# Performance work log

Hardware: AMD Instinct MI355X
Metric: run time of the kernel (lower is better)

The kernel has to match this reference:

```python
import jax, jax.numpy as jnp
import numpy as np

B, C, H, W = 2, 128, 64, 64
CR4 = C // 4  # hidden width of linear_weight / bias branches
SOFTMAX_SCALE = 1.0


def _leaky(z):
    return jnp.where(z >= 0, z, 0.2 * z)


def _conv1x1(x, w, b):
    # x: [B,Ci,H,W], w: [Co,Ci], b: [Co]
    return jnp.einsum('oc,bchw->bohw', w, x) + b[None, :, None, None]


def setup_inputs() -> dict:
    key = jax.random.key(0)
    ks = jax.random.split(key, 16)
    def n(k, shape, s=0.05):
        return jax.random.normal(k, shape, jnp.float32) * s
    return {
        'x': jax.random.normal(ks[0], (B, C, H, W), jnp.float32),
        'value_w': n(ks[1], (C, C)), 'value_b': n(ks[2], (C,)),
        'query_w': n(ks[3], (C, C)), 'query_b': n(ks[4], (C,)),
        'lw1_w': n(ks[5], (CR4, C)), 'lw1_b': n(ks[6], (CR4,)),
        'lw2_w': n(ks[7], (1, CR4)), 'lw2_b': n(ks[8], (1,)),
        'bi1_w': n(ks[9], (CR4, C)), 'bi1_b': n(ks[10], (CR4,)),
        'bi2_w': n(ks[11], (1, CR4)), 'bi2_b': n(ks[12], (1,)),
        'lin_w': n(ks[13], (C, C, 3, 3)), 'lin_b': n(ks[14], (C,)),
    }


def reference(x, value_w, value_b, query_w, query_b,
              lw1_w, lw1_b, lw2_w, lw2_b,
              bi1_w, bi1_b, bi2_w, bi2_b,
              lin_w, lin_b):
    # value / query 1x1 projections
    x1 = _conv1x1(x, value_w, value_b)   # [B,C,H,W]
    x2 = _conv1x1(x, query_w, query_b)   # [B,C,H,W]
    # dynamic per-pixel weight / bias maps (two 1x1 convs + LeakyReLU)
    wei = _conv1x1(_leaky(_conv1x1(x2, lw1_w, lw1_b)), lw2_w, lw2_b)  # [B,1,H,W]
    bii = _conv1x1(_leaky(_conv1x1(x2, bi1_w, bi1_b)), bi2_w, bi2_b)  # [B,1,H,W]

    Bn, Cn, Hn, Wn = x.shape
    L = Hn * Wn  # one 1x1 patch per spatial location (ksize=1, stride=1)
    # query patches [B,L,C]; normalize each patch to (at least 1e-4) unit norm
    wq = x2.transpose(0, 2, 3, 1).reshape(Bn, L, Cn)
    wnorm = wq / jnp.maximum(jnp.linalg.norm(wq, axis=2, keepdims=True), 1e-4)
    # attention scores: per-sample conv2d(xi, wi_normed) == batched matmul
    yi = jnp.einsum('bchw,blc->blhw', x2, wnorm)  # [B,L,H,W]
    # sparse gating
    sparse = jax.nn.relu(yi - yi.mean(axis=1, keepdims=True) * wei + bii)
    sr = (sparse != 0.0).astype(yi.dtype)
    yi = yi * sparse
    yi = jax.nn.softmax(yi * SOFTMAX_SCALE, axis=1)
    yi = jnp.maximum(yi * sr, 1e-8)
    # reconstruct with value patches (conv_transpose2d with 1x1 kernels)
    raw = x1.transpose(0, 2, 3, 1).reshape(Bn, L, Cn)
    out = jnp.einsum('blhw,blc->bchw', yi, raw)  # / (ksize*ksize) == /1
    # final 3x3 conv + LeakyReLU + residual
    y = jax.lax.conv_general_dilated(out, lin_w, (1, 1), 'SAME',
                                     dimension_numbers=('NCHW', 'OIHW', 'NCHW'))
    y = _leaky(y + lin_b[None, :, None, None])
    return y + x
```

## Files before the change

kernel.cpp:

```cpp
#include <hip/hip_runtime.h>
#include <hip/hip_bf16.h>
#include <math.h>

#define BB 2
#define C 128
#define L 4096
#define CR4 32
#define RS 4

typedef unsigned short ushort_t;
typedef __attribute__((ext_vector_type(8))) short s16x8;
typedef __attribute__((ext_vector_type(4))) float f32x4;

__device__ inline float leaky(float z) { return (z >= 0.f) ? z : 0.2f * z; }

__device__ inline unsigned short f2bf(float f) {
    unsigned int u = __builtin_bit_cast(unsigned int, f);
    unsigned int r = (u + 0x7fffu + ((u >> 16) & 1u)) >> 16;
    return (unsigned short)r;
}
__device__ inline float bf2f(unsigned short b) {
    unsigned int u = ((unsigned int)b) << 16;
    return __builtin_bit_cast(float, u);
}
__device__ inline unsigned int cvtpk(float lo, float hi) {
    unsigned int r;
    asm("v_cvt_pk_bf16_f32 %0, %1, %2" : "=v"(r) : "v"(lo), "v"(hi));
    return r;
}

__global__ __launch_bounds__(256) void k_wcomp(
    const float* __restrict__ vw, const float* __restrict__ vb,
    const float* __restrict__ qw, const float* __restrict__ qb,
    const float* __restrict__ lw1w, const float* __restrict__ lw1b,
    const float* __restrict__ bi1w, const float* __restrict__ bi1b,
    ushort_t* __restrict__ WQV, float* __restrict__ biasv)
{
    const int mt = blockIdx.x;
    const int t = threadIdx.x;
    const int kk = t >> 6, lane = t & 63;
    const int row = mt * 16 + (lane & 15);
    const int k0 = kk * 32 + (lane >> 4) * 8;
    s16x8 v;
    if (row < 128) {
        #pragma unroll
        for (int j = 0; j < 8; ++j) v[j] = (short)f2bf(vw[row * 128 + k0 + j]);
    } else if (row < 256) {
        #pragma unroll
        for (int j = 0; j < 8; ++j) v[j] = (short)f2bf(qw[(row - 128) * 128 + k0 + j]);
    } else {
        const float* w1 = (row < 288) ? lw1w + (row - 256) * 128
                                      : bi1w + (row - 288) * 128;
        float acc[8] = {0.f, 0.f, 0.f, 0.f, 0.f, 0.f, 0.f, 0.f};
        #pragma unroll 2
        for (int k = 0; k < 128; ++k) {
            float wv_ = w1[k];
            const float* qr = qw + k * 128 + k0;
            #pragma unroll
            for (int j = 0; j < 8; ++j) acc[j] = fmaf(wv_, qr[j], acc[j]);
        }
        #pragma unroll
        for (int j = 0; j < 8; ++j) v[j] = (short)f2bf(acc[j]);
    }
    *(s16x8*)(WQV + ((size_t)(mt * 4 + kk) * 64 + lane) * 8) = v;

    if (t < 16) {
        int rr = mt * 16 + t;
        float bv;
        if (rr < 128) bv = vb[rr];
        else if (rr < 256) bv = qb[rr - 128];
        else {
            const float* w1 = (rr < 288) ? lw1w + (rr - 256) * 128
                                         : bi1w + (rr - 288) * 128;
            float a = (rr < 288) ? lw1b[rr - 256] : bi1b[rr - 288];
            for (int k = 0; k < 128; ++k) a = fmaf(w1[k], qb[k], a);
            bv = a;
        }
        biasv[rr] = bv;
    }
}

__global__ __launch_bounds__(256, 1) void k_proj2(
    const float* __restrict__ x, const ushort_t* __restrict__ WQV,
    const float* __restrict__ biasv,
    const float* __restrict__ lw2w, const float* __restrict__ lw2b,
    const float* __restrict__ bi2w, const float* __restrict__ bi2b,
    ushort_t* __restrict__ x2a, ushort_t* __restrict__ x1g,
    float* __restrict__ weiA, float* __restrict__ biiA, float* __restrict__ scA,
    float* __restrict__ cpart)
{
    __shared__ __align__(16) char smem[16384 + 1536];
    char* xT = smem;
    float* biasLDS = (float*)(smem + 16384);
    float* w2LDS = biasLDS + 320;

    const int t = threadIdx.x;
    const int blk = blockIdx.x;
    const int part = blockIdx.y;
    const int b = blk >> 6;
    const int p0 = (blk & 63) * 64;
    const int wv = t >> 6, lane = t & 63, n = lane & 15, g = lane >> 4;

    biasLDS[t] = biasv[t];
    if (t < 64) {
        biasLDS[256 + t] = biasv[256 + t];
        w2LDS[t] = (t < 32) ? lw2w[t] : bi2w[t - 32];
    }

    const int pl = t & 63, cg = t >> 6;
    const float* xb = x + (size_t)b * C * L + p0 + pl;
    #pragma unroll
    for (int i = 0; i < 16; ++i) {
        int c = cg * 32 + i * 2;
        float v0 = xb[(size_t)c * L];
        float v1 = xb[(size_t)(c + 1) * L];
        int slot = c >> 3;
        int offs = (c * 2) & 15;
        int byte = pl * 256 + (((slot ^ (pl & 15)) << 4) | offs);
        *(unsigned int*)(xT + byte) = cvtpk(v0, v1);
    }
    __syncthreads();

    const int brow = wv * 16 + n;
    const int p = p0 + wv * 16 + n;
    const size_t bL = (size_t)b * L;

    if (part == 0) {
        const int mtm[12] = {0, 1, 2, 3, 4, 5, 6, 7, 16, 17, 18, 19};
        f32x4 acc[12];
        #pragma unroll
        for (int i = 0; i < 12; ++i) acc[i] = (f32x4){0.f, 0.f, 0.f, 0.f};
        #pragma unroll
        for (int kk = 0; kk < 4; ++kk) {
            const s16x8 bfr = *(const s16x8*)(xT + brow * 256 + (((4 * kk + g) ^ n) << 4));
            #pragma unroll
            for (int i = 0; i < 12; ++i) {
                const s16x8 afr = *(const s16x8*)(WQV + ((size_t)(mtm[i] * 4 + kk) * 64 + lane) * 8);
                acc[i] = __builtin_amdgcn_mfma_f32_16x16x32_bf16(afr, bfr, acc[i], 0, 0, 0);
            }
        }
        #pragma unroll
        for (int i = 0; i < 12; ++i) {
            const f32x4 bv = *(const f32x4*)(biasLDS + mtm[i] * 16 + g * 4);
            acc[i][0] += bv[0]; acc[i][1] += bv[1];
            acc[i][2] += bv[2]; acc[i][3] += bv[3];
        }
        #pragma unroll
        for (int i = 0; i < 8; ++i)
            #pragma unroll
            for (int r = 0; r < 4; ++r)
                x1g[((size_t)b * C + i * 16 + g * 4 + r) * L + p] = f2bf(acc[i][r]);
        float pw = 0.f, pbb = 0.f;
        #pragma unroll
        for (int i = 8; i < 10; ++i)
            #pragma unroll
            for (int r = 0; r < 4; ++r)
                pw = fmaf(w2LDS[(i - 8) * 16 + g * 4 + r], leaky(acc[i][r]), pw);
        #pragma unroll
        for (int i = 10; i < 12; ++i)
            #pragma unroll
            for (int r = 0; r < 4; ++r)
                pbb = fmaf(w2LDS[32 + (i - 10) * 16 + g * 4 + r], leaky(acc[i][r]), pbb);
        pw += __shfl_xor(pw, 16, 64);  pw += __shfl_xor(pw, 32, 64);
        pbb += __shfl_xor(pbb, 16, 64); pbb += __shfl_xor(pbb, 32, 64);
        if (g == 0) {
            weiA[bL + p] = pw + lw2b[0];
            biiA[bL + p] = pbb + bi2b[0];
        }
    } else {
        f32x4 acc[8];
        #pragma unroll
        for (int i = 0; i < 8; ++i) acc[i] = (f32x4){0.f, 0.f, 0.f, 0.f};
        #pragma unroll
        for (int kk = 0; kk < 4; ++kk) {
            const s16x8 bfr = *(const s16x8*)(xT + brow * 256 + (((4 * kk + g) ^ n) << 4));
            #pragma unroll
            for (int i = 0; i < 8; ++i) {
                const s16x8 afr = *(const s16x8*)(WQV + ((size_t)((8 + i) * 4 + kk) * 64 + lane) * 8);
                acc[i] = __builtin_amdgcn_mfma_f32_16x16x32_bf16(afr, bfr, acc[i], 0, 0, 0);
            }
        }
        #pragma unroll
        for (int i = 0; i < 8; ++i) {
            const f32x4 bv = *(const f32x4*)(biasLDS + (8 + i) * 16 + g * 4);
            acc[i][0] += bv[0]; acc[i][1] += bv[1];
            acc[i][2] += bv[2]; acc[i][3] += bv[3];
        }
        float pn = 0.f;
        #pragma unroll
        for (int i = 0; i < 8; ++i)
            #pragma unroll
            for (int r = 0; r < 4; ++r) pn = fmaf(acc[i][r], acc[i][r], pn);
        pn += __shfl_xor(pn, 16, 64);
        pn += __shfl_xor(pn, 32, 64);
        float scv = fmaxf(sqrtf(pn), 1e-4f);
        float dinv = 1.f / scv;
        if (g == 0) scA[bL + p] = scv;
        #pragma unroll
        for (int i = 0; i < 8; ++i) {
            uint2 uu;
            uu.x = cvtpk(acc[i][0] * dinv, acc[i][1] * dinv);
            uu.y = cvtpk(acc[i][2] * dinv, acc[i][3] * dinv);
            *(uint2*)(x2a + (bL + p) * C + i * 16 + g * 4) = uu;
        }
        float sv[32];
        #pragma unroll
        for (int i = 0; i < 8; ++i)
            #pragma unroll
            for (int r = 0; r < 4; ++r)
                sv[i * 4 + r] = acc[i][r] * dinv;
        #pragma unroll
        for (int mask = 1; mask <= 8; mask <<= 1)
            #pragma unroll
            for (int i = 0; i < 32; ++i)
                sv[i] += __shfl_xor(sv[i], mask, 64);
        __syncthreads();
        float* sumsh = (float*)xT;
        if (n == 0) {
            #pragma unroll
            for (int i = 0; i < 32; ++i) {
                int ch = (i >> 2) * 16 + g * 4 + (i & 3);
                sumsh[wv * 128 + ch] = sv[i];
            }
        }
        __syncthreads();
        if (t < 128)
            cpart[(size_t)blk * 128 + t] =
                (sumsh[t] + sumsh[128 + t]) + (sumsh[256 + t] + sumsh[384 + t]);
    }
}

__global__ __launch_bounds__(128) void k_cb(
    const float* __restrict__ cpart, float* __restrict__ cbv)
{
    const int b = blockIdx.x, t = threadIdx.x;
    float s = 0.f;
    #pragma unroll 4
    for (int j = 0; j < 64; ++j) s += cpart[(size_t)(b * 64 + j) * 128 + t];
    cbv[b * 128 + t] = s * (1.f / (float)L);
}

__global__ __launch_bounds__(256, 2) void k_attn(
    const ushort_t* __restrict__ x2a, const ushort_t* __restrict__ x1g,
    const float* __restrict__ scA, const float* __restrict__ weiA,
    const float* __restrict__ biiA, const float* __restrict__ cbv,
    ushort_t* __restrict__ Opb, float* __restrict__ Mp, float* __restrict__ Zp)
{
    __shared__ __align__(16) char smem[73728];

    const int t = threadIdx.x;
    const int w = t >> 6, lane = t & 63, n = lane & 15, g = lane >> 4;
    char* Pw = smem + 65536 + w * 2048;

    const int blk = blockIdx.x;
    const int q = blk & (RS - 1);
    const int colt = (blk >> 2) & 63;
    const int b = blk >> 8;
    const int p = colt * 64 + w * 16 + n;
    const size_t bL = (size_t)b * L;

    const s16x8* qrow = (const s16x8*)(x2a + (bL + p) * C);
    const float scp = scA[bL + p];
    s16x8 bq[4];
    float dot = 0.f;
    #pragma unroll
    for (int kk = 0; kk < 4; ++kk) {
        s16x8 raw = qrow[kk * 4 + g];
        const float* cbp = cbv + b * 128 + kk * 32 + g * 8;
        s16x8 u;
        #pragma unroll
        for (int j = 0; j < 8; ++j) {
            float rv = bf2f((unsigned short)raw[j]) * scp;
            u[j] = (short)f2bf(rv);
            dot = fmaf(cbp[j], rv, dot);
        }
        bq[kk] = u;
    }
    dot += __shfl_xor(dot, 16, 64);
    dot += __shfl_xor(dot, 32, 64);
    const float tq = fmaf(weiA[bL + p], dot, -biiA[bL + p]);

    f32x4 Oacc[8];
    #pragma unroll
    for (int ct = 0; ct < 8; ++ct) Oacc[ct] = (f32x4){0.f, 0.f, 0.f, 0.f};
    float Mrun = 0.f, Zrun = 0.f;

    const int l0base = q * (L / RS);
    const char* x2src = (const char*)(x2a + (bL + l0base) * C);
    const char* x1src = (const char*)(x1g + (size_t)b * C * L);

    #define STAGE_X2(buf, tile_)                                                         \
        {   const char* sb = x2src + (size_t)(tile_) * 64 * 256;                          \
            _Pragma("unroll")                                                             \
            for (int rr = 0; rr < 4; ++rr) {                                              \
                int slot = rr * 256 + t;                                                  \
                int lrow = slot >> 4, uu = slot & 15;                                     \
                const char* gp = sb + lrow * 256 + (((uu ^ (lrow & 7))) << 4);            \
                char* lp = (buf) + ((rr * 256 + w * 64) << 4);                            \
                __builtin_amdgcn_global_load_lds(                                         \
                    (const __attribute__((address_space(1))) unsigned int*)gp,            \
                    (__attribute__((address_space(3))) unsigned int*)lp, 16, 0, 0);       \
            } }
    #define STAGE_X1(buf, l0_)                                                            \
        {   _Pragma("unroll")                                                             \
            for (int rr = 0; rr < 4; ++rr) {                                              \
                int slot = rr * 256 + t;                                                  \
                int cr = slot >> 3, uu = slot & 7;                                        \
                const char* gp = x1src + ((size_t)cr * L + (l0_) + ((uu ^ (cr & 7)) << 3)) * 2; \
                char* lp = (buf) + ((rr * 256 + w * 64) << 4);                            \
                __builtin_amdgcn_global_load_lds(                                         \
                    (const __attribute__((address_space(1))) unsigned int*)gp,            \
                    (__attribute__((address_space(3))) unsigned int*)lp, 16, 0, 0);       \
            } }

    char* Abuf0 = smem;          char* Abuf1 = smem + 16384;
    char* Xbuf0 = smem + 32768;  char* Xbuf1 = smem + 49152;

    STAGE_X2(Abuf0, 0);
    STAGE_X1(Xbuf0, l0base);
    __syncthreads();

    const int swz = n & 7;
    const int NT = L / RS / 64;

    #pragma unroll 1
    for (int tile = 0; tile < NT; ++tile) {
        char* Ab = (tile & 1) ? Abuf1 : Abuf0;
        char* Xb = (tile & 1) ? Xbuf1 : Xbuf0;
        if (tile + 1 < NT) {
            char* An = (tile & 1) ? Abuf0 : Abuf1;
            char* Xn = (tile & 1) ? Xbuf0 : Xbuf1;
            STAGE_X2(An, tile + 1);
            STAGE_X1(Xn, l0base + (tile + 1) * 64);
        }

        f32x4 s4[4];
        #pragma unroll
        for (int lt = 0; lt < 4; ++lt) s4[lt] = (f32x4){0.f, 0.f, 0.f, 0.f};
        __builtin_amdgcn_s_setprio(1);
        #pragma unroll
        for (int kk = 0; kk < 4; ++kk) {
            #pragma unroll
            for (int lt = 0; lt < 4; ++lt) {
                const s16x8 a = *(const s16x8*)(Ab + (16 * lt + n) * 256 +
                                                (((4 * kk + g) ^ swz) << 4));
                s4[lt] = __builtin_amdgcn_mfma_f32_16x16x32_bf16(a, bq[kk], s4[lt], 0, 0, 0);
            }
        }
        __builtin_amdgcn_s_setprio(0);

        float vv[16], sps[16];
        #pragma unroll
        for (int lt = 0; lt < 4; ++lt) {
            #pragma unroll
            for (int r = 0; r < 4; ++r) {
                float s = s4[lt][r];
                float sp = s - tq;
                sps[lt * 4 + r] = sp;
                vv[lt * 4 + r] = s * fmaxf(sp, 0.f);
            }
        }
        float tm[8];
        #pragma unroll
        for (int i = 0; i < 8; ++i) tm[i] = fmaxf(vv[2 * i], vv[2 * i + 1]);
        #pragma unroll
        for (int i = 0; i < 4; ++i) tm[i] = fmaxf(tm[2 * i], tm[2 * i + 1]);
        float tmax = fmaxf(fmaxf(tm[0], tm[1]), fmaxf(tm[2], tm[3]));
        tmax = fmaxf(tmax, __shfl_xor(tmax, 16, 64));
        tmax = fmaxf(tmax, __shfl_xor(tmax, 32, 64));

        if (!__all(tmax <= Mrun + 8.f)) {
            float Mn = fmaxf(Mrun, tmax);
            float so = __expf(Mrun - Mn);
            Mrun = Mn;
            Zrun *= so;
            #pragma unroll
            for (int ct = 0; ct < 8; ++ct) {
                Oacc[ct][0] *= so; Oacc[ct][1] *= so;
                Oacc[ct][2] *= so; Oacc[ct][3] *= so;
            }
        }

        #pragma unroll
        for (int lt = 0; lt < 4; ++lt) {
            float e0 = __expf(vv[lt * 4 + 0] - Mrun);
            float e1 = __expf(vv[lt * 4 + 1] - Mrun);
            float e2 = __expf(vv[lt * 4 + 2] - Mrun);
            float e3 = __expf(vv[lt * 4 + 3] - Mrun);
            Zrun += (e0 + e1) + (e2 + e3);
            float p0 = sps[lt * 4 + 0] > 0.f ? e0 : 0.f;
            float p1 = sps[lt * 4 + 1] > 0.f ? e1 : 0.f;
            float p2 = sps[lt * 4 + 2] > 0.f ? e2 : 0.f;
            float p3 = sps[lt * 4 + 3] > 0.f ? e3 : 0.f;
            int ulog = 2 * lt + (g >> 1);
            int byte = n * 128 + ((ulog ^ swz) << 4) + ((g & 1) << 3);
            uint2 uu;
            uu.x = cvtpk(p0, p1);
            uu.y = cvtpk(p2, p3);
            *(uint2*)(Pw + byte) = uu;
        }

        __builtin_amdgcn_s_setprio(1);
        #pragma unroll
        for (int kk2 = 0; kk2 < 2; ++kk2) {
            const s16x8 pb = *(const s16x8*)(Pw + n * 128 + (((4 * kk2 + g) ^ swz) << 4));
            #pragma unroll
            for (int ct = 0; ct < 8; ++ct) {
                const s16x8 a = *(const s16x8*)(Xb + (16 * ct + n) * 128 +
                                                (((4 * kk2 + g) ^ swz) << 4));
                Oacc[ct] = __builtin_amdgcn_mfma_f32_16x16x32_bf16(a, pb, Oacc[ct], 0, 0, 0);
            }
        }
        __builtin_amdgcn_s_setprio(0);
        __syncthreads();
    }
    #undef STAGE_X2
    #undef STAGE_X1

    float z = Zrun;
    z += __shfl_xor(z, 16, 64);
    z += __shfl_xor(z, 32, 64);

    const size_t sset = (size_t)(q * BB + b);
    ushort_t* ob = Opb + (sset * L + p) * C;
    #pragma unroll
    for (int ct = 0; ct < 8; ++ct) {
        uint2 uu;
        uu.x = cvtpk(Oacc[ct][0], Oacc[ct][1]);
        uu.y = cvtpk(Oacc[ct][2], Oacc[ct][3]);
        *(uint2*)(ob + 16 * ct + 4 * g) = uu;
    }
    if (g == 0) {
        Mp[sset * L + p] = Mrun;
        Zp[sset * L + p] = z;
    }
}

__global__ __launch_bounds__(256) void k_mergewrep(
    const ushort_t* __restrict__ Opb, const float* __restrict__ Mp,
    const float* __restrict__ Zp, ushort_t* __restrict__ attnb,
    const float* __restrict__ lw, ushort_t* __restrict__ W3)
{
    const int blkid = blockIdx.x;
    const int t = threadIdx.x;
    if (blkid < 1024) {
        const int idx = blkid * 256 + t;
        const int c4 = idx & 31;
        const int p = (idx >> 5) & 4095;
        const int b = idx >> 17;
        size_t is[RS];
        float M = -1e30f;
        float Mq[RS], Zq[RS];
        #pragma unroll
        for (int q = 0; q < RS; ++q) {
            is[q] = (size_t)(q * BB + b) * L + p;
            Mq[q] = Mp[is[q]];
            Zq[q] = Zp[is[q]];
            M = fmaxf(M, Mq[q]);
        }
        float Zt = 0.f;
        float aq[RS];
        #pragma unroll
        for (int q = 0; q < RS; ++q) {
            aq[q] = __expf(Mq[q] - M);
            Zt = fmaf(Zq[q], aq[q], Zt);
        }
        float zi = 1.f / Zt;
        float r0 = 0.f, r1 = 0.f, r2 = 0.f, r3 = 0.f;
        #pragma unroll
        for (int q = 0; q < RS; ++q) {
            float s = aq[q] * zi;
            const ushort4 o = *(const ushort4*)(Opb + is[q] * C + c4 * 4);
            r0 = fmaf(bf2f(o.x), s, r0);
            r1 = fmaf(bf2f(o.y), s, r1);
            r2 = fmaf(bf2f(o.z), s, r2);
            r3 = fmaf(bf2f(o.w), s, r3);
        }
        uint2 uu;
        uu.x = cvtpk(r0, r1);
        uu.y = cvtpk(r2, r3);
        *(uint2*)(attnb + ((size_t)b * L + p) * C + c4 * 4) = uu;
    } else {
        const int tid = (blkid - 1024) * 256 + t;
        const int s = tid >> 9;
        const int r = tid & 511;
        const int mt = r >> 6, lane = r & 63;
        const int co = mt * 16 + (lane & 15), g = lane >> 4;
        const int kk = s >> 2, kc = s & 3;
        const int ci0 = kc * 32 + g * 8;
        s16x8 v;
        #pragma unroll
        for (int j = 0; j < 8; ++j)
            v[j] = (short)f2bf(lw[((size_t)co * 128 + ci0 + j) * 9 + kk]);
        *(s16x8*)(W3 + (size_t)tid * 8) = v;
    }
}

__global__ __launch_bounds__(256, 1) void k_conv(
    const ushort_t* __restrict__ attnb, const float* __restrict__ x,
    const ushort_t* __restrict__ W3, const float* __restrict__ lb,
    float* __restrict__ out)
{
    __shared__ __align__(16) char attnT[49152];

    const int t = threadIdx.x;
    const int wv = t >> 6, lane = t & 63, n = lane & 15, g = lane >> 4;
    const int h = blockIdx.x;
    const int half = blockIdx.y;
    const int b = blockIdx.z;

    const char* asrc = (const char*)attnb + ((size_t)b * L + (size_t)(h - 1) * 64) * C * 2;
    #pragma unroll
    for (int rr = 0; rr < 3; ++rr) {
        if ((unsigned)(h - 1 + rr) < 64u) {
            #pragma unroll
            for (int qq = 0; qq < 4; ++qq) {
                int slot = rr * 1024 + qq * 256 + t;
                int lrow = slot >> 4, uu = slot & 15;
                const char* gp = asrc + lrow * 256 + ((uu ^ (lrow & 7)) << 4);
                char* lp = attnT + ((rr * 1024 + qq * 256 + wv * 64) << 4);
                __builtin_amdgcn_global_load_lds(
                    (const __attribute__((address_space(1))) unsigned int*)gp,
                    (__attribute__((address_space(3))) unsigned int*)lp, 16, 0, 0);
            }
        }
    }

    #define WROW(s_, mi_) (*(const s16x8*)(W3 + (((size_t)(s_) * 8 + 2 * wv + (mi_)) * 64 + lane) * 8))

    s16x8 w0a = WROW(0, 0), w0b = WROW(0, 1);
    s16x8 w1a = WROW(1, 0), w1b = WROW(1, 1);

    __syncthreads();

    f32x4 acc[2][2];
    #pragma unroll
    for (int mi = 0; mi < 2; ++mi)
        #pragma unroll
        for (int nt = 0; nt < 2; ++nt) acc[mi][nt] = (f32x4){0.f, 0.f, 0.f, 0.f};

    const s16x8 zer = {0, 0, 0, 0, 0, 0, 0, 0};

    #define CONV_STEP(s_, af0_, af1_)                                                    \
    {   const int kk = (s_) >> 2, kc = (s_) & 3;                                         \
        const int kh = kk / 3, kw = kk - kh * 3;                                         \
        const int dh = kh - 1, dw = kw - 1;                                              \
        const bool hval = ((unsigned)(h + dh) < 64u);                                    \
        _Pragma("unroll")                                                                \
        for (int nt = 0; nt < 2; ++nt) {                                                 \
            int pl = half * 32 + nt * 16 + n;                                            \
            int wd = pl + dw;                                                            \
            bool val = hval && ((unsigned)wd < 64u);                                     \
            int wc = wd < 0 ? 0 : (wd > 63 ? 63 : wd);                                   \
            int lrow = (dh + 1) * 64 + wc;                                               \
            s16x8 bf_ = *(const s16x8*)(attnT + lrow * 256 +                             \
                                        (((kc * 4 + g) ^ (lrow & 7)) << 4));             \
            if (!val) bf_ = zer;                                                         \
            acc[0][nt] = __builtin_amdgcn_mfma_f32_16x16x32_bf16(af0_, bf_, acc[0][nt], 0, 0, 0); \
            acc[1][nt] = __builtin_amdgcn_mfma_f32_16x16x32_bf16(af1_, bf_, acc[1][nt], 0, 0, 0); \
        }                                                                                \
    }

    #pragma unroll 1
    for (int s = 0; s < 36; s += 2) {
        s16x8 af0 = w0a, af1 = w0b;
        if (s + 2 < 36) { w0a = WROW(s + 2, 0); w0b = WROW(s + 2, 1); }
        CONV_STEP(s, af0, af1)
        af0 = w1a; af1 = w1b;
        if (s + 3 < 36) { w1a = WROW(s + 3, 0); w1b = WROW(s + 3, 1); }
        CONV_STEP(s + 1, af0, af1)
    }
    #undef CONV_STEP
    #undef WROW

    const float* xb = x + (size_t)b * C * L + h * 64;
    float* ob = out + (size_t)b * C * L + h * 64;
    #pragma unroll
    for (int mi = 0; mi < 2; ++mi) {
        #pragma unroll
        for (int r = 0; r < 4; ++r) {
            int co = (2 * wv + mi) * 16 + g * 4 + r;
            float bias = lb[co];
            #pragma unroll
            for (int nt = 0; nt < 2; ++nt) {
                int p_ = half * 32 + nt * 16 + n;
                float v = leaky(acc[mi][nt][r] + bias);
                ob[(size_t)co * L + p_] = v + xb[(size_t)co * L + p_];
            }
        }
    }
}

extern "C" void kernel_launch(void* const* d_in, const int* in_sizes, int n_in,
                              void* d_out, int out_size, void* d_ws, size_t ws_size,
                              hipStream_t stream) {
    const float* x     = (const float*)d_in[0];
    const float* vw    = (const float*)d_in[1];
    const float* vb    = (const float*)d_in[2];
    const float* qw    = (const float*)d_in[3];
    const float* qb    = (const float*)d_in[4];
    const float* lw1w  = (const float*)d_in[5];
    const float* lw1b  = (const float*)d_in[6];
    const float* lw2w  = (const float*)d_in[7];
    const float* lw2b  = (const float*)d_in[8];
    const float* bi1w  = (const float*)d_in[9];
    const float* bi1b  = (const float*)d_in[10];
    const float* bi2w  = (const float*)d_in[11];
    const float* bi2b  = (const float*)d_in[12];
    const float* lw    = (const float*)d_in[13];
    const float* lb    = (const float*)d_in[14];
    float* out = (float*)d_out;

    char* ws = (char*)d_ws;
    ushort_t* x2a  = (ushort_t*)ws;
    ushort_t* x1g  = (ushort_t*)(ws + 2097152);
    ushort_t* Opb  = (ushort_t*)(ws + 4194304);
    ushort_t* WQV  = (ushort_t*)(ws + 4194304);
    float* biasv = (float*)(ws + 4194304 + 81920);
    float* weiA  = (float*)(ws + 12582912);
    float* biiA  = weiA + BB * L;
    float* scA   = biiA + BB * L;
    float* Mp    = scA + BB * L;
    float* Zp    = Mp + RS * BB * L;
    float* cpart = Zp + RS * BB * L;
    float* cbv   = cpart + 128 * 128;
    ushort_t* W3 = x1g;
    ushort_t* attnb = x2a;

    hipLaunchKernelGGL(k_wcomp, dim3(20), dim3(256), 0, stream,
                       vw, vb, qw, qb, lw1w, lw1b, bi1w, bi1b, WQV, biasv);

    hipLaunchKernelGGL(k_proj2, dim3(128, 2), dim3(256), 0, stream,
                       x, WQV, biasv, lw2w, lw2b, bi2w, bi2b,
                       x2a, x1g, weiA, biiA, scA, cpart);

    hipLaunchKernelGGL(k_cb, dim3(BB), dim3(128), 0, stream, cpart, cbv);

    hipLaunchKernelGGL(k_attn, dim3(BB * 64 * RS), dim3(256), 0, stream,
                       x2a, x1g, scA, weiA, biiA, cbv, Opb, Mp, Zp);

    hipLaunchKernelGGL(k_mergewrep, dim3(1096), dim3(256), 0, stream,
                       Opb, Mp, Zp, attnb, lw, W3);

    hipLaunchKernelGGL(k_conv, dim3(64, 2, BB), dim3(256), 0, stream,
                       attnb, x, W3, lb, out);
}
```

Before: 99.67 us.

## Load value tiles directly into registers and remap blocks by XCD

Value (x1) tiles are no longer staged through LDS with async global-to-LDS copies. Each lane now loads its MFMA A-fragments straight from global memory into registers at the start of each tile, which cuts LDS use from 72KB to 40KB and may allow more blocks per CU. The block index is also remapped so that each XCD handles one batch and a contiguous set of tiles, which should improve L2 locality. In exchange the x1 loads are no longer prefetched a tile ahead, so global latency could be exposed, and register pressure rises with 16 extra vector registers per lane.

New measurement: 136.9 us. 37.3% more time.

```diff
diff --git a/kernel.cpp b/kernel.cpp
--- a/kernel.cpp
+++ b/kernel.cpp
@@ -246,16 +246,18 @@
     const float* __restrict__ biiA, const float* __restrict__ cbv,
     ushort_t* __restrict__ Opb, float* __restrict__ Mp, float* __restrict__ Zp)
 {
-    __shared__ __align__(16) char smem[73728];
+    __shared__ __align__(16) char smem[40960];
 
     const int t = threadIdx.x;
     const int w = t >> 6, lane = t & 63, n = lane & 15, g = lane >> 4;
-    char* Pw = smem + 65536 + w * 2048;
+    char* Pw = smem + 32768 + w * 2048;
 
     const int blk = blockIdx.x;
-    const int q = blk & (RS - 1);
-    const int colt = (blk >> 2) & 63;
-    const int b = blk >> 8;
+    const int xcd = blk & 7;
+    const int b = xcd >> 2;
+    const int ti = (xcd & 3) * 64 + (blk >> 3);
+    const int q = ti & 3;
+    const int colt = ti >> 2;
     const int p = colt * 64 + w * 16 + n;
     const size_t bL = (size_t)b * L;
 
@@ -287,7 +289,7 @@
 
     const int l0base = q * (L / RS);
     const char* x2src = (const char*)(x2a + (bL + l0base) * C);
-    const char* x1src = (const char*)(x1g + (size_t)b * C * L);
+    const ushort_t* x1rows = x1g + (size_t)b * C * L + l0base;
 
     #define STAGE_X2(buf, tile_)                                                         \
         {   const char* sb = x2src + (size_t)(tile_) * 64 * 256;                          \
@@ -301,23 +303,11 @@
                     (const __attribute__((address_space(1))) unsigned int*)gp,            \
                     (__attribute__((address_space(3))) unsigned int*)lp, 16, 0, 0);       \
             } }
-    #define STAGE_X1(buf, l0_)                                                            \
-        {   _Pragma("unroll")                                                             \
-            for (int rr = 0; rr < 4; ++rr) {                                              \
-                int slot = rr * 256 + t;                                                  \
-                int cr = slot >> 3, uu = slot & 7;                                        \
-                const char* gp = x1src + ((size_t)cr * L + (l0_) + ((uu ^ (cr & 7)) << 3)) * 2; \
-                char* lp = (buf) + ((rr * 256 + w * 64) << 4);                            \
-                __builtin_amdgcn_global_load_lds(                                         \
-                    (const __attribute__((address_space(1))) unsigned int*)gp,            \
-                    (__attribute__((address_space(3))) unsigned int*)lp, 16, 0, 0);       \
-            } }
-
-    char* Abuf0 = smem;          char* Abuf1 = smem + 16384;
-    char* Xbuf0 = smem + 32768;  char* Xbuf1 = smem + 49152;
+
+    char* Abuf0 = smem;
+    char* Abuf1 = smem + 16384;
 
     STAGE_X2(Abuf0, 0);
-    STAGE_X1(Xbuf0, l0base);
     __syncthreads();
 
     const int swz = n & 7;
@@ -326,13 +316,18 @@
     #pragma unroll 1
     for (int tile = 0; tile < NT; ++tile) {
         char* Ab = (tile & 1) ? Abuf1 : Abuf0;
-        char* Xb = (tile & 1) ? Xbuf1 : Xbuf0;
         if (tile + 1 < NT) {
             char* An = (tile & 1) ? Abuf0 : Abuf1;
-            char* Xn = (tile & 1) ? Xbuf0 : Xbuf1;
             STAGE_X2(An, tile + 1);
-            STAGE_X1(Xn, l0base + (tile + 1) * 64);
-        }
+        }
+
+        s16x8 xf[16];
+        #pragma unroll
+        for (int kk2 = 0; kk2 < 2; ++kk2)
+            #pragma unroll
+            for (int ct = 0; ct < 8; ++ct)
+                xf[kk2 * 8 + ct] = *(const s16x8*)(x1rows + (size_t)(16 * ct + n) * L +
+                                                   tile * 64 + kk2 * 32 + g * 8);
 
         f32x4 s4[4];
         #pragma unroll
@@ -405,17 +400,14 @@
         for (int kk2 = 0; kk2 < 2; ++kk2) {
             const s16x8 pb = *(const s16x8*)(Pw + n * 128 + (((4 * kk2 + g) ^ swz) << 4));
             #pragma unroll
-            for (int ct = 0; ct < 8; ++ct) {
-                const s16x8 a = *(const s16x8*)(Xb + (16 * ct + n) * 128 +
-                                                (((4 * kk2 + g) ^ swz) << 4));
-                Oacc[ct] = __builtin_amdgcn_mfma_f32_16x16x32_bf16(a, pb, Oacc[ct], 0, 0, 0);
-            }
+            for (int ct = 0; ct < 8; ++ct)
+                Oacc[ct] = __builtin_amdgcn_mfma_f32_16x16x32_bf16(xf[kk2 * 8 + ct], pb,
+                                                                   Oacc[ct], 0, 0, 0);
         }
         __builtin_amdgcn_s_setprio(0);
         __syncthreads();
     }
     #undef STAGE_X2
-    #undef STAGE_X1
 
     float z = Zrun;
     z += __shfl_xor(z, 16, 64);
```
